# Kernel optimization log

Hardware: AMD Instinct MI355X
Metric: run time of the kernel (lower is better)

## Reference

```python
import jax, jax.numpy as jnp
import numpy as np
from functools import partial

B, S, A = 128, 256, 8
V, E, H, C, HOPS = 50000, 300, 300, 3, 3

def _lstm_dir(x, lens, Wih, Whh, bih, bhh):
    # x: [B,S,E]; masked (packed-style) LSTM: padded steps don't update state, output 0
    b, s, _ = x.shape
    h_dim = Whh.shape[1]
    xg = jnp.einsum('bse,ge->bsg', x, Wih) + bih  # [B,S,4H]
    mask = (jnp.arange(s)[None, :] < lens[:, None])  # [B,S]

    def step(carry, inp):
        h, c = carry
        xg_t, m = inp  # [B,4H], [B]
        g = xg_t + h @ Whh.T + bhh
        i, f, gg, o = jnp.split(g, 4, axis=-1)
        i = jax.nn.sigmoid(i); f = jax.nn.sigmoid(f)
        gg = jnp.tanh(gg); o = jax.nn.sigmoid(o)
        c_new = f * c + i * gg
        h_new = o * jnp.tanh(c_new)
        m2 = m[:, None]
        h2 = jnp.where(m2, h_new, h)
        c2 = jnp.where(m2, c_new, c)
        out = jnp.where(m2, h_new, 0.0)
        return (h2, c2), out

    z = jnp.zeros((b, h_dim), x.dtype)
    _, outs = jax.lax.scan(step, (z, z), (xg.transpose(1, 0, 2), mask.T))
    return outs.transpose(1, 0, 2)

def _bilstm(x, lens, Wih_f, Whh_f, bih_f, bhh_f, Wih_b, Whh_b, bih_b, bhh_b):
    out_f = _lstm_dir(x, lens, Wih_f, Whh_f, bih_f, bhh_f)
    s = x.shape[1]
    t = jnp.arange(s)[None, :]
    # reverse each sequence within its own valid length
    idx = jnp.where(t < lens[:, None], lens[:, None] - 1 - t, t)  # [B,S]
    x_rev = jnp.take_along_axis(x, idx[:, :, None], axis=1)
    out_b_rev = _lstm_dir(x_rev, lens, Wih_b, Whh_b, bih_b, bhh_b)
    out_b = jnp.take_along_axis(out_b_rev, idx[:, :, None], axis=1)
    return jnp.concatenate([out_f, out_b], axis=-1)  # [B,S,2H]

def _locationed_memory(memory, mem_len, left_len, asp_len):
    b, s, _ = memory.shape
    pos = jnp.arange(s, dtype=memory.dtype)[None, :]  # [1,S]
    ml = mem_len[:, None].astype(memory.dtype)
    ll = left_len[:, None].astype(memory.dtype)
    al = asp_len[:, None].astype(memory.dtype)
    in_left = pos < ll
    in_right = (pos >= ll + al) & (pos < ml)
    w = jnp.where(in_left, 1.0 - (ll - pos) / ml,
        jnp.where(in_right, 1.0 - (pos - ll - al + 1.0) / ml, 1.0))
    u = jnp.where(in_left, pos - ll,
        jnp.where(in_right, pos - ll - al + 1.0, 0.0))
    v = memory * w[:, :, None]
    return jnp.concatenate([v, u[:, :, None]], axis=2)  # [B,S,2H+1]

def _gru_cell(x, h, Wih, Whh, bih, bhh):
    gi = x @ Wih.T + bih
    gh = h @ Whh.T + bhh
    i_r, i_z, i_n = jnp.split(gi, 3, axis=-1)
    h_r, h_z, h_n = jnp.split(gh, 3, axis=-1)
    r = jax.nn.sigmoid(i_r + h_r)
    z = jax.nn.sigmoid(i_z + h_z)
    n = jnp.tanh(i_n + r * h_n)
    return (1.0 - z) * n + z * h

def setup_inputs() -> dict:
    key = jax.random.key(0)
    ks = jax.random.split(key, 24)
    mem_len = jax.random.randint(ks[0], (B,), S // 2, S + 1)
    asp_len = jax.random.randint(ks[1], (B,), 1, A + 1)
    max_left = mem_len - asp_len
    left_len = jax.random.randint(ks[2], (B,), 0, 10**6) % (max_left + 1)

    def make_ids(k, n, lens):
        tok = jax.random.randint(k, (B, n), 1, V)
        return jnp.where(jnp.arange(n)[None, :] < lens[:, None], tok, 0)

    text = make_ids(ks[3], S, mem_len)
    aspect = make_ids(ks[4], A, asp_len)
    left_context = make_ids(ks[5], S, left_len)

    def nrm(k, shape, scale=0.05):
        return jax.random.normal(k, shape, jnp.float32) * scale

    params = dict(
        embedding=nrm(ks[6], (V, E), 0.1),
        Wih_f=nrm(ks[7], (4 * H, E)), Whh_f=nrm(ks[8], (4 * H, H)),
        bih_f=nrm(ks[9], (4 * H,)), bhh_f=nrm(ks[10], (4 * H,)),
        Wih_b=nrm(ks[11], (4 * H, E)), Whh_b=nrm(ks[12], (4 * H, H)),
        bih_b=nrm(ks[13], (4 * H,)), bhh_b=nrm(ks[14], (4 * H,)),
        att_W=nrm(ks[15], (1, 2 * H + 1 + 2 * E)), att_b=nrm(ks[16], (1,)),
        gru_Wih=nrm(ks[17], (3 * E, 2 * H + 1)), gru_Whh=nrm(ks[18], (3 * E, E)),
        gru_bih=nrm(ks[19], (3 * E,)), gru_bhh=nrm(ks[20], (3 * E,)),
        dense_W=nrm(ks[21], (C, E)), dense_b=nrm(ks[22], (C,)),
    )
    return dict(text=text, aspect=aspect, left_context=left_context, **params)

def reference(text, aspect, left_context, embedding,
              Wih_f, Whh_f, bih_f, bhh_f, Wih_b, Whh_b, bih_b, bhh_b,
              att_W, att_b, gru_Wih, gru_Whh, gru_bih, gru_bhh,
              dense_W, dense_b):
    left_len = jnp.sum(left_context != 0, axis=-1)
    mem_len = jnp.sum(text != 0, axis=-1)
    asp_len = jnp.sum(aspect != 0, axis=-1)

    memory = embedding[text]  # [B,S,E]
    memory = _bilstm(memory, mem_len, Wih_f, Whh_f, bih_f, bhh_f,
                     Wih_b, Whh_b, bih_b, bhh_b)  # [B,S,2H]
    memory = _locationed_memory(memory, mem_len, left_len, asp_len)  # [B,S,2H+1]

    asp_emb = jnp.sum(embedding[aspect], axis=1) / asp_len[:, None].astype(jnp.float32)  # [B,E]

    et = jnp.zeros_like(asp_emb)
    b, s, _ = memory.shape
    for _ in range(HOPS):
        a = jnp.concatenate([
            memory,
            jnp.broadcast_to(et[:, None, :], (b, s, et.shape[-1])),
            jnp.broadcast_to(asp_emb[:, None, :], (b, s, asp_emb.shape[-1])),
        ], axis=-1)  # [B,S,2H+1+2E]
        g = jnp.einsum('bsd,od->bso', a, att_W) + att_b  # [B,S,1]
        alpha = jax.nn.softmax(g, axis=1)
        i = jnp.einsum('bso,bsd->bd', alpha, memory)  # [B,2H+1]
        et = _gru_cell(i, et, gru_Wih, gru_Whh, gru_bih, gru_bhh)
    return et @ dense_W.T + dense_b  # [B,C]
```

## Files before the change

### kernel.cpp

```cpp
#include <hip/hip_runtime.h>
#include <hip/hip_bf16.h>
#include <math.h>

#define B_ 128
#define S_ 256
#define A_ 8
#define E_ 300
#define H_ 300
#define KPAD 320
#define NGU 16
#define NCOL 80
#define WROW 648
#define HROW 328
#define NBLK 128

typedef unsigned short u16;
typedef unsigned int u32;
typedef unsigned long long u64;
typedef __attribute__((ext_vector_type(8))) short short8;
typedef __attribute__((ext_vector_type(4))) float floatx4;
typedef __attribute__((ext_vector_type(4))) unsigned int u32x4;

#define MFMA16(a, b, c) __builtin_amdgcn_mfma_f32_16x16x32_bf16((a), (b), (c), 0, 0, 0)

__device__ __host__ __forceinline__ int gu_cnt(int g) { return g < 6 ? 20 : 18; }
__device__ __host__ __forceinline__ int gu_u0(int g) { return g < 6 ? 20 * g : 120 + 18 * (g - 6); }

static constexpr size_t oLens = 0;
static constexpr size_t oFlg  = 1536;
static constexpr size_t oH    = 4096;
static constexpr size_t oMemX = 331776;
static constexpr size_t oWp   = 42274816;
static constexpr size_t oBp   = 45551616;
static constexpr size_t oMemV = 45561856;
static constexpr size_t oIT   = 124205056;
static constexpr size_t oGi   = 124512768;
static constexpr size_t oGh   = 124973568;
static constexpr size_t oEt   = 125434368;
static constexpr size_t oSc   = 125587968;
static constexpr size_t oMirr = 125719040;
static constexpr size_t oHL2  = 125721088;
static constexpr size_t WS_NEED = 126048768;

__device__ __forceinline__ u16 f2bf(float f) {
  union { float f; unsigned u; } v; v.f = f;
  unsigned r = (v.u + 0x7FFFu + ((v.u >> 16) & 1u)) >> 16;
  return (u16)r;
}
__device__ __forceinline__ float sigm(float x) { return 1.f / (1.f + __expf(-x)); }
__device__ __forceinline__ float tanh_f(float x) {
  x = fminf(15.f, fmaxf(-15.f, x));
  float e = __expf(2.f * x);
  return (e - 1.f) / (e + 1.f);
}
__device__ __forceinline__ u32 ld_sc0(const u32* p) {
  u32 v;
  asm volatile("global_load_dword %0, %1, off sc0\n\ts_waitcnt vmcnt(0)"
               : "=v"(v) : "v"(p) : "memory");
  return v;
}

__global__ __launch_bounds__(256) void init_kernel(const int* __restrict__ text,
                                                   const int* __restrict__ aspect,
                                                   const int* __restrict__ leftc,
                                                   char* __restrict__ ws) {
  const int bid = blockIdx.x, tid = threadIdx.x;
  if (bid == 0) {
    if (tid < B_) {
      int c = 0; const int* p = text + tid * S_;
      for (int s = 0; s < S_; ++s) c += (p[s] != 0);
      ((int*)(ws + oLens))[tid] = c;
    }
  } else if (bid == 1) {
    if (tid < B_) {
      int c = 0; const int* p = leftc + tid * S_;
      for (int s = 0; s < S_; ++s) c += (p[s] != 0);
      ((int*)(ws + oLens + 512))[tid] = c;
    }
  } else if (bid == 2) {
    if (tid < B_) {
      int c = 0; const int* p = aspect + tid * A_;
      for (int s = 0; s < A_; ++s) c += (p[s] != 0);
      ((int*)(ws + oLens + 1024))[tid] = c;
    }
  } else {
    const int F1 = 512, F2 = 512, HW = 81920, H2 = 81920, EW = 38400;
    const int total = F1 + F2 + HW + H2 + EW;
    for (int i = (bid - 3) * 256 + tid; i < total; i += 64 * 256) {
      int j = i;
      if (j < F1)            { ((u32*)(ws + oFlg))[j] = 0u; continue; }  j -= F1;
      if (j < F2)            { ((u32*)(ws + oMirr))[j] = 0u; continue; } j -= F2;
      if (j < HW)            { ((u32*)(ws + oH))[j] = 0u; continue; }    j -= HW;
      if (j < H2)            { ((u32*)(ws + oHL2))[j] = 0u; continue; }  j -= H2;
      ((u32*)(ws + oEt))[j] = 0u;
    }
  }
}

__global__ __launch_bounds__(256) void pack_kernel(
    const float* __restrict__ WihF, const float* __restrict__ WhhF,
    const float* __restrict__ bihF, const float* __restrict__ bhhF,
    const float* __restrict__ WihB, const float* __restrict__ WhhB,
    const float* __restrict__ bihB, const float* __restrict__ bhhB,
    char* __restrict__ ws) {
  const int WTOT = 2 * NGU * NCOL * 640;
  int idx = blockIdx.x * 256 + threadIdx.x;
  if (idx < WTOT) {
    int k = idx % 640;
    int n = (idx / 640) % NCOL;
    int g = (idx / (640 * NCOL)) % NGU;
    int dir = idx / (640 * NCOL * NGU);
    float v = 0.f;
    const int cnt = gu_cnt(g), u0 = gu_u0(g);
    if (n < cnt * 4) {
      int col = (n & 3) * 300 + u0 + (n >> 2);
      const float* Wih = dir ? WihB : WihF;
      const float* Whh = dir ? WhhB : WhhF;
      if (k < 300)                  v = Wih[(size_t)col * 300 + k];
      else if (k >= 320 && k < 620) v = Whh[(size_t)col * 300 + (k - 320)];
    }
    ((u16*)(ws + oWp))[idx] = f2bf(v);
  } else {
    int j = idx - WTOT;
    if (j < 2 * NGU * NCOL) {
      int n = j % NCOL; int g = (j / NCOL) % NGU; int dir = j / (NCOL * NGU);
      float v = 0.f;
      const int cnt = gu_cnt(g), u0 = gu_u0(g);
      if (n < cnt * 4) {
        int col = (n & 3) * 300 + u0 + (n >> 2);
        v = (dir ? bihB : bihF)[col] + (dir ? bhhB : bhhF)[col];
      }
      ((float*)(ws + oBp))[j] = v;
    }
  }
}

__global__ __launch_bounds__(KPAD) void gather_kernel(const int* __restrict__ text,
                                                      const float* __restrict__ emb,
                                                      char* __restrict__ ws) {
  const int bid = blockIdx.x;
  const int t = bid & 255;
  const int b = (bid >> 8) & 127;
  const int dir = bid >> 15;
  const int len = ((const int*)(ws + oLens))[b];
  const int tp = (dir == 0) ? t : ((t < len) ? (len - 1 - t) : t);
  const int tok = text[b * S_ + tp];
  u16* dst = (u16*)(ws + oMemX) + ((size_t)((dir * B_ + b) * S_ + t)) * KPAD;
  const float* src = emb + (size_t)tok * E_;
  const int k = threadIdx.x;
  float v = (k < E_) ? src[k] : 0.f;
  dst[k] = f2bf(v);
}

__global__ __launch_bounds__(256, 1) void lstm_kernel(char* __restrict__ ws) {
  const int bid = (int)blockIdx.x;
  const int pod = bid & 7;
  const int dir = pod >> 2;
  const int gb  = pod & 3;
  const int g   = bid >> 3;
  const int cnt = gu_cnt(g), u0 = gu_u0(g);
  const int npair = cnt >> 1;
  const int tid = threadIdx.x;
  const int wv = tid >> 6;
  const int lane = tid & 63;
  const int quad = lane >> 4;
  const int l16 = lane & 15;
  const int Mtile = wv >> 1;
  const int nt0 = (wv & 1) ? 3 : 0;
  const int ntc = (wv & 1) ? 2 : 3;

  const u64* __restrict__ Wp64 = (const u64*)(ws + oWp) + (size_t)(dir * NGU + g) * NCOL * 160;
  const float* __restrict__ Bpk = (const float*)(ws + oBp) + (dir * NGU + g) * NCOL;
  const u16* __restrict__ memx = (const u16*)(ws + oMemX) + (size_t)dir * B_ * S_ * KPAD;
  const u16* __restrict__ hb16 = (const u16*)(ws + oH);
  u32* __restrict__ hb32 = (u32*)(ws + oH);
  const u16* __restrict__ hl16 = (const u16*)(ws + oHL2);
  u32* __restrict__ hl32 = (u32*)(ws + oHL2);
  float* __restrict__ memv = (float*)(ws + oMemV);
  u32* __restrict__ flagsP = (u32*)(ws + oFlg) + (size_t)pod * 64;
  u32* __restrict__ flagsM = (u32*)(ws + oMirr) + (size_t)pod * 64;

  __shared__ __align__(16) u16 Wlds[NCOL * WROW];
  __shared__ __align__(16) u16 hLds[32 * HROW];
  __shared__ float gatesLds[32 * 81];
  __shared__ float cS[640];
  __shared__ float hS[640];
  __shared__ float biasS[NCOL];
  __shared__ int lenS[32], llS[32], alS[32];
  __shared__ int remoteS;

  for (int i = tid; i < NCOL * 160; i += 256) {
    int n = i / 160, k4 = i - n * 160;
    ((u64*)Wlds)[n * 162 + k4] = Wp64[i];
  }
  for (int i = tid; i < 640; i += 256) { cS[i] = 0.f; hS[i] = 0.f; }
  if (tid < NCOL) biasS[tid] = Bpk[tid];
  if (tid < 32) {
    lenS[tid] = ((const int*)(ws + oLens))[gb * 32 + tid];
    llS[tid]  = ((const int*)(ws + oLens + 512))[gb * 32 + tid];
    alS[tid]  = ((const int*)(ws + oLens + 1024))[gb * 32 + tid];
  }
  if (tid == 0) remoteS = 0;
  __syncthreads();

  const int row = gb * 32 + Mtile * 16 + l16;
  const u16* wq = Wlds + l16 * WROW + quad * 8;

  int eoff[5]; u16* ldst[5];
  #pragma unroll
  for (int it = 0; it < 5; ++it) {
    int e = (it * 256 + tid) * 8;
    int r = e / KPAD, c = e - r * KPAD;
    eoff[it] = e;
    ldst[it] = hLds + r * HROW + c;
  }
  const u16* hA = hLds + (Mtile * 16 + l16) * HROW + quad * 8;

  short8 xv[10];
  {
    const u16* xr = memx + ((size_t)row * S_) * KPAD + quad * 8;
    #pragma unroll
    for (int kk = 0; kk < 10; ++kk) xv[kk] = *(const short8*)(xr + kk * 32);
  }

  for (int t = 0; t < S_; ++t) {
    if (t > 0) {
      if (wv == 0) {
        const u32 target = (u32)t;
        int spin = 0;
        while (true) {
          u32 f = 0xFFFFFFFFu;
          const int rm = *(volatile int*)&remoteS;
          if (lane < NGU)
            f = rm ? __hip_atomic_load(&flagsM[lane * 4], __ATOMIC_RELAXED, __HIP_MEMORY_SCOPE_AGENT)
                   : ld_sc0(&flagsP[lane * 4]);
          if (__all((int)(f >= target))) break;
          ++spin;
          if (!rm && spin > 64 && (spin & 15) == 0) {
            u32 fm = 0u, fp = 0xFFFFFFFFu;
            if (lane < NGU) {
              fm = __hip_atomic_load(&flagsM[lane * 4], __ATOMIC_RELAXED, __HIP_MEMORY_SCOPE_AGENT);
              fp = ld_sc0(&flagsP[lane * 4]);
            }
            if (__any((int)(fm > fp))) { if (lane == 0) *(volatile int*)&remoteS = 1; }
          }
          if (rm) __builtin_amdgcn_s_sleep(1);
        }
      }
      __syncthreads();
      __builtin_amdgcn_fence(__ATOMIC_ACQUIRE, "workgroup");
    }

    const int rem = *(volatile int*)&remoteS;
    u32x4 hstash[5];
    {
      const size_t pbase = (((size_t)(t & 1) * 2 + dir) * B_ + gb * 32) * KPAD;
      if (rem) {
        const u16* hpan = hb16 + pbase;
        #pragma unroll
        for (int it = 0; it < 5; ++it)
          asm volatile("global_load_dwordx4 %0, %1, off sc1"
                       : "=v"(hstash[it]) : "v"(hpan + eoff[it]) : "memory");
      } else {
        const u16* hpan = hl16 + pbase;
        #pragma unroll
        for (int it = 0; it < 5; ++it)
          asm volatile("global_load_dwordx4 %0, %1, off sc0"
                       : "=v"(hstash[it]) : "v"(hpan + eoff[it]) : "memory");
      }
    }

    floatx4 acc[3];
    acc[0] = (floatx4){0.f, 0.f, 0.f, 0.f}; acc[1] = acc[0]; acc[2] = acc[0];
    #pragma unroll
    for (int kk = 0; kk < 10; ++kk) {
      const int ko = kk * 32;
      #pragma unroll
      for (int j = 0; j < 3; ++j) {
        if (j < ntc)
          acc[j] = MFMA16(xv[kk], *(const short8*)(wq + (nt0 + j) * 16 * WROW + ko), acc[j]);
      }
    }

    asm volatile("s_waitcnt vmcnt(0)" ::: "memory");
    #pragma unroll
    for (int it = 0; it < 5; ++it) *(u32x4*)ldst[it] = hstash[it];
    __syncthreads();

    #pragma unroll
    for (int kk = 0; kk < 10; ++kk) {
      const short8 av = *(const short8*)(hA + kk * 32);
      const int ko = 320 + kk * 32;
      #pragma unroll
      for (int j = 0; j < 3; ++j) {
        if (j < ntc)
          acc[j] = MFMA16(av, *(const short8*)(wq + (nt0 + j) * 16 * WROW + ko), acc[j]);
      }
    }

    #pragma unroll
    for (int j = 0; j < 3; ++j) {
      if (j < ntc) {
        const int colb = (nt0 + j) * 16 + l16;
        const int rb = Mtile * 16 + quad * 4;
        #pragma unroll
        for (int r = 0; r < 4; ++r)
          gatesLds[(rb + r) * 81 + colb] = acc[j][r];
      }
    }
    __syncthreads();

    const int nxt = (t + 1) & 1;
    float2 sv[2]; float* sa[2]; bool sval[2];
    #pragma unroll
    for (int z = 0; z < 2; ++z) {
      const int it = tid + z * 256;
      sval[z] = (it < 32 * npair);
      if (!sval[z]) continue;
      const int bl = it & 31;
      const int pl = it >> 5;
      const int ul0 = pl * 2;
      const int len = lenS[bl];
      const bool m = (t < len);
      const float* gp = gatesLds + bl * 81 + ul0 * 4;
      const float* bp = biasS + ul0 * 4;
      float h0K, h1K, h0N, h1N;
      {
        float ig = sigm(gp[0] + bp[0]);
        float fg = sigm(gp[1] + bp[1]);
        float gt = tanh_f(gp[2] + bp[2]);
        float og = sigm(gp[3] + bp[3]);
        float cOld = cS[ul0 * 32 + bl], hOld = hS[ul0 * 32 + bl];
        float cNew = fg * cOld + ig * gt;
        float hNew = og * tanh_f(cNew);
        cS[ul0 * 32 + bl] = m ? cNew : cOld;
        h0K = m ? hNew : hOld;
        hS[ul0 * 32 + bl] = h0K;
        h0N = m ? hNew : 0.f;
      }
      {
        float ig = sigm(gp[4] + bp[4]);
        float fg = sigm(gp[5] + bp[5]);
        float gt = tanh_f(gp[6] + bp[6]);
        float og = sigm(gp[7] + bp[7]);
        float cOld = cS[(ul0 + 1) * 32 + bl], hOld = hS[(ul0 + 1) * 32 + bl];
        float cNew = fg * cOld + ig * gt;
        float hNew = og * tanh_f(cNew);
        cS[(ul0 + 1) * 32 + bl] = m ? cNew : cOld;
        h1K = m ? hNew : hOld;
        hS[(ul0 + 1) * 32 + bl] = h1K;
        h1N = m ? hNew : 0.f;
      }
      const int bglob = gb * 32 + bl;
      const size_t hidx = (((size_t)nxt * 2 + dir) * B_ + bglob) * 160 + ((u0 + ul0) >> 1);
      u32 packed = (u32)f2bf(h0K) | ((u32)f2bf(h1K) << 16);
      hl32[hidx] = packed;
      __hip_atomic_store(&hb32[hidx], packed,
                         __ATOMIC_RELAXED, __HIP_MEMORY_SCOPE_AGENT);
      int pos = (dir == 0) ? t : (m ? (len - 1 - t) : t);
      float ml = (float)len, ll = (float)llS[bl], al = (float)alS[bl];
      float p = (float)pos;
      float wl;
      if (p < ll) wl = 1.f - (ll - p) / ml;
      else if ((p >= ll + al) && (p < ml)) wl = 1.f - (p - ll - al + 1.f) / ml;
      else wl = 1.f;
      sv[z] = make_float2(h0N * wl, h1N * wl);
      sa[z] = &memv[((size_t)bglob * S_ + pos) * 600 + dir * 300 + u0 + ul0];
    }

    __builtin_amdgcn_fence(__ATOMIC_RELEASE, "workgroup");
    __syncthreads();
    if (tid == 0) {
      *(volatile u32*)&flagsP[g * 4] = (u32)(t + 1);
      __hip_atomic_store(&flagsM[g * 4], (u32)(t + 1),
                         __ATOMIC_RELAXED, __HIP_MEMORY_SCOPE_AGENT);
    }

    #pragma unroll
    for (int z = 0; z < 2; ++z)
      if (sval[z]) *(float2*)sa[z] = sv[z];
    if (t + 1 < S_) {
      const u16* xr = memx + ((size_t)row * S_ + (t + 1)) * KPAD + quad * 8;
      #pragma unroll
      for (int kk = 0; kk < 10; ++kk) xv[kk] = *(const short8*)(xr + kk * 32);
    }
  }
}

__global__ __launch_bounds__(256) void score_kernel(const float* __restrict__ attW,
                                                    char* __restrict__ ws) {
  const int bid = blockIdx.x;
  const int b = bid >> 1, sh = bid & 1;
  const int tid = threadIdx.x, wv = tid >> 6, lane = tid & 63;
  __shared__ float aW[601];
  for (int i = tid; i < 601; i += 256) aW[i] = attW[i];
  const float* memv = (const float*)(ws + oMemV) + (size_t)b * S_ * 600;
  const float ml = (float)((const int*)(ws + oLens))[b];
  const float ll = (float)((const int*)(ws + oLens + 512))[b];
  const float al = (float)((const int*)(ws + oLens + 1024))[b];
  __syncthreads();
  float* scg = (float*)(ws + oSc) + b * S_;
  for (int s = sh * 128 + wv; s < sh * 128 + 128; s += 4) {
    const float* rowp = memv + (size_t)s * 600;
    float acc = 0.f;
    for (int d = lane; d < 600; d += 64) acc += rowp[d] * aW[d];
    for (int off = 32; off; off >>= 1) acc += __shfl_xor(acc, off);
    if (lane == 0) {
      float p = (float)s;
      bool inl = p < ll;
      bool inr = (p >= ll + al) && (p < ml);
      float u = inl ? (p - ll) : (inr ? (p - ll - al + 1.f) : 0.f);
      scg[s] = acc + u * aW[600];
    }
  }
}

__global__ __launch_bounds__(256) void attn_kernel(char* __restrict__ ws) {
  const int bid = blockIdx.x;
  const int b = bid >> 1, dh = bid & 1;
  const int tid = threadIdx.x, wv = tid >> 6, lane = tid & 63;
  __shared__ float alpha[256];
  __shared__ float red[8];
  const float* scg = (const float*)(ws + oSc) + b * S_;
  float v = scg[tid];
  float mx = v;
  for (int off = 32; off; off >>= 1) mx = fmaxf(mx, __shfl_xor(mx, off));
  if (lane == 0) red[wv] = mx;
  __syncthreads();
  mx = fmaxf(fmaxf(red[0], red[1]), fmaxf(red[2], red[3]));
  float e = __expf(v - mx);
  float sm = e;
  for (int off = 32; off; off >>= 1) sm += __shfl_xor(sm, off);
  if (lane == 0) red[4 + wv] = sm;
  __syncthreads();
  float tot = red[4] + red[5] + red[6] + red[7];
  alpha[tid] = e / tot;
  const float ml = (float)((const int*)(ws + oLens))[b];
  const float ll = (float)((const int*)(ws + oLens + 512))[b];
  const float al = (float)((const int*)(ws + oLens + 1024))[b];
  __syncthreads();
  const float* memv = (const float*)(ws + oMemV) + (size_t)b * S_ * 600;
  float* iT = (float*)(ws + oIT);
  const int d0 = dh * 301, d1 = dh ? 601 : 301;
  for (int d = d0 + tid; d < d1; d += 256) {
    float acc = 0.f;
    if (d < 600) {
      for (int s = 0; s < 256; ++s) acc += alpha[s] * memv[(size_t)s * 600 + d];
    } else {
      for (int s = 0; s < 256; ++s) {
        float p = (float)s;
        bool inl = p < ll;
        bool inr = (p >= ll + al) && (p < ml);
        float u = inl ? (p - ll) : (inr ? (p - ll - al + 1.f) : 0.f);
        acc += alpha[s] * u;
      }
    }
    iT[d * 128 + b] = acc;
  }
}

__global__ __launch_bounds__(256) void gi_kernel(const float* __restrict__ Wih,
                                                 const float* __restrict__ bih,
                                                 char* __restrict__ ws) {
  int idx = blockIdx.x * 256 + threadIdx.x;
  int r = idx >> 7, b = idx & 127;
  if (r >= 900) return;
  const float* iT = (const float*)(ws + oIT);
  const float* wr = Wih + (size_t)r * 601;
  float acc = bih[r];
  for (int d = 0; d < 601; ++d) acc += iT[d * 128 + b] * wr[d];
  ((float*)(ws + oGi))[r * 128 + b] = acc;
}

__global__ __launch_bounds__(256) void gh_kernel(const float* __restrict__ Whh,
                                                 const float* __restrict__ bhh,
                                                 char* __restrict__ ws) {
  int idx = blockIdx.x * 256 + threadIdx.x;
  int r = idx >> 7, b = idx & 127;
  if (r >= 900) return;
  const float* et = (const float*)(ws + oEt);
  const float* wr = Whh + (size_t)r * 300;
  float acc = bhh[r];
  for (int u = 0; u < 300; ++u) acc += et[u * 128 + b] * wr[u];
  ((float*)(ws + oGh))[r * 128 + b] = acc;
}

__global__ __launch_bounds__(256) void up_kernel(char* __restrict__ ws) {
  int idx = blockIdx.x * 256 + threadIdx.x;
  int u = idx >> 7, b = idx & 127;
  if (u >= 300) return;
  const float* gi = (const float*)(ws + oGi);
  const float* gh = (const float*)(ws + oGh);
  float* et = (float*)(ws + oEt);
  float rr = sigm(gi[u * 128 + b] + gh[u * 128 + b]);
  float zz = sigm(gi[(300 + u) * 128 + b] + gh[(300 + u) * 128 + b]);
  float nn = tanh_f(gi[(600 + u) * 128 + b] + rr * gh[(600 + u) * 128 + b]);
  float old = et[u * 128 + b];
  et[u * 128 + b] = (1.f - zz) * nn + zz * old;
}

__global__ __launch_bounds__(384) void dense_kernel(const float* __restrict__ dW,
                                                    const float* __restrict__ dB,
                                                    float* __restrict__ out,
                                                    const char* __restrict__ ws) {
  int tid = threadIdx.x;
  if (tid >= 384) return;
  int b = tid / 3, c = tid - 3 * (tid / 3);
  const float* et = (const float*)(ws + oEt);
  float acc = dB[c];
  const float* wr = dW + c * 300;
  for (int u = 0; u < 300; ++u) acc += et[u * 128 + b] * wr[u];
  out[b * 3 + c] = acc;
}

extern "C" void kernel_launch(void* const* d_in, const int* in_sizes, int n_in,
                              void* d_out, int out_size, void* d_ws, size_t ws_size,
                              hipStream_t stream) {
  const int* text = (const int*)d_in[0];
  const int* aspect = (const int*)d_in[1];
  const int* leftc = (const int*)d_in[2];
  const float* emb = (const float*)d_in[3];
  const float* WihF = (const float*)d_in[4];
  const float* WhhF = (const float*)d_in[5];
  const float* bihF = (const float*)d_in[6];
  const float* bhhF = (const float*)d_in[7];
  const float* WihB = (const float*)d_in[8];
  const float* WhhB = (const float*)d_in[9];
  const float* bihB = (const float*)d_in[10];
  const float* bhhB = (const float*)d_in[11];
  const float* attW = (const float*)d_in[12];
  const float* gruWih = (const float*)d_in[14];
  const float* gruWhh = (const float*)d_in[15];
  const float* gruBih = (const float*)d_in[16];
  const float* gruBhh = (const float*)d_in[17];
  const float* denseW = (const float*)d_in[18];
  const float* denseB = (const float*)d_in[19];
  float* out = (float*)d_out;
  char* ws = (char*)d_ws;
  if (ws_size < WS_NEED) return;

  init_kernel<<<67, 256, 0, stream>>>(text, aspect, leftc, ws);
  pack_kernel<<<6420, 256, 0, stream>>>(WihF, WhhF, bihF, bhhF, WihB, WhhB, bihB, bhhB, ws);
  gather_kernel<<<2 * B_ * S_, KPAD, 0, stream>>>(text, emb, ws);
  lstm_kernel<<<NBLK, 256, 0, stream>>>(ws);
  score_kernel<<<2 * B_, 256, 0, stream>>>(attW, ws);
  attn_kernel<<<2 * B_, 256, 0, stream>>>(ws);
  gi_kernel<<<450, 256, 0, stream>>>(gruWih, gruBih, ws);
  for (int h = 0; h < 3; ++h) {
    gh_kernel<<<450, 256, 0, stream>>>(gruWhh, gruBhh, ws);
    up_kernel<<<150, 256, 0, stream>>>(ws);
  }
  dense_kernel<<<1, 384, 0, stream>>>(denseW, denseB, out, ws);
}
```

Baseline: 1.912 ms.

## Replace per-step flag synchronization with step-tagged hidden-state exchange

Removes the separate flag arrays and the flag spin-wait between LSTM recurrence blocks. Each hidden-state word is now written as a 64-bit value carrying the step tag, and consumers poll the data itself until every tag matches, so the release fence, the extra barrier and the flag round trip disappear from each timestep. It also changes the gate LDS stride and replaces __syncthreads with raw barriers. The cost is doubled hidden-state traffic and repeated reloads of whole panels while spinning, and correctness depends on 64-bit stores being seen atomically.

```diff
diff --git a/kernel.cpp b/kernel.cpp
--- a/kernel.cpp
+++ b/kernel.cpp
@@ -13,6 +13,8 @@
 #define WROW 648
 #define HROW 328
 #define NBLK 128
+#define GST 82
+#define PROBE_START 256
 
 typedef unsigned short u16;
 typedef unsigned int u32;
@@ -22,13 +24,12 @@
 typedef __attribute__((ext_vector_type(4))) unsigned int u32x4;
 
 #define MFMA16(a, b, c) __builtin_amdgcn_mfma_f32_16x16x32_bf16((a), (b), (c), 0, 0, 0)
+#define LD4_SC0(d, a) asm volatile("global_load_dwordx4 %0, %1, off sc0" : "=v"(d) : "v"(a) : "memory")
 
 __device__ __host__ __forceinline__ int gu_cnt(int g) { return g < 6 ? 20 : 18; }
 __device__ __host__ __forceinline__ int gu_u0(int g) { return g < 6 ? 20 * g : 120 + 18 * (g - 6); }
 
 static constexpr size_t oLens = 0;
-static constexpr size_t oFlg  = 1536;
-static constexpr size_t oH    = 4096;
 static constexpr size_t oMemX = 331776;
 static constexpr size_t oWp   = 42274816;
 static constexpr size_t oBp   = 45551616;
@@ -38,9 +39,9 @@
 static constexpr size_t oGh   = 124973568;
 static constexpr size_t oEt   = 125434368;
 static constexpr size_t oSc   = 125587968;
-static constexpr size_t oMirr = 125719040;
-static constexpr size_t oHL2  = 125721088;
-static constexpr size_t WS_NEED = 126048768;
+static constexpr size_t oHTP  = 125719040;
+static constexpr size_t oHTS  = 126374400;
+static constexpr size_t WS_NEED = 127029760;
 
 __device__ __forceinline__ u16 f2bf(float f) {
   union { float f; unsigned u; } v; v.f = f;
@@ -53,11 +54,27 @@
   float e = __expf(2.f * x);
   return (e - 1.f) / (e + 1.f);
 }
-__device__ __forceinline__ u32 ld_sc0(const u32* p) {
-  u32 v;
-  asm volatile("global_load_dword %0, %1, off sc0\n\ts_waitcnt vmcnt(0)"
-               : "=v"(v) : "v"(p) : "memory");
-  return v;
+
+__device__ __forceinline__ bool tags_ok(const u32x4 (&q)[10], u32 tgv, int scol0) {
+  bool ok = true;
+  #pragma unroll
+  for (int i = 0; i < 10; ++i) {
+    ok = ok && ((q[i][1] == tgv) || (scol0 + 2 * i >= 150));
+    ok = ok && ((q[i][3] == tgv) || (scol0 + 2 * i + 1 >= 150));
+  }
+  return ok;
+}
+__device__ __forceinline__ void load_plain(u32x4 (&q)[10], const u64* sp) {
+  #pragma unroll
+  for (int i = 0; i < 10; ++i) LD4_SC0(q[i], sp + 2 * i);
+}
+__device__ __forceinline__ void load_mirror(u32x4 (&q)[10], const u64* sp) {
+  #pragma unroll
+  for (int i = 0; i < 10; ++i) {
+    u64 lo = __hip_atomic_load(sp + 2 * i, __ATOMIC_RELAXED, __HIP_MEMORY_SCOPE_AGENT);
+    u64 hi = __hip_atomic_load(sp + 2 * i + 1, __ATOMIC_RELAXED, __HIP_MEMORY_SCOPE_AGENT);
+    q[i] = (u32x4){(u32)lo, (u32)(lo >> 32), (u32)hi, (u32)(hi >> 32)};
+  }
 }
 
 __global__ __launch_bounds__(256) void init_kernel(const int* __restrict__ text,
@@ -84,14 +101,12 @@
       ((int*)(ws + oLens + 1024))[tid] = c;
     }
   } else {
-    const int F1 = 512, F2 = 512, HW = 81920, H2 = 81920, EW = 38400;
-    const int total = F1 + F2 + HW + H2 + EW;
+    const int T1 = 163840, T2 = 163840, EW = 38400;
+    const int total = T1 + T2 + EW;
     for (int i = (bid - 3) * 256 + tid; i < total; i += 64 * 256) {
       int j = i;
-      if (j < F1)            { ((u32*)(ws + oFlg))[j] = 0u; continue; }  j -= F1;
-      if (j < F2)            { ((u32*)(ws + oMirr))[j] = 0u; continue; } j -= F2;
-      if (j < HW)            { ((u32*)(ws + oH))[j] = 0u; continue; }    j -= HW;
-      if (j < H2)            { ((u32*)(ws + oHL2))[j] = 0u; continue; }  j -= H2;
+      if (j < T1)            { ((u32*)(ws + oHTP))[j] = 0u; continue; }  j -= T1;
+      if (j < T2)            { ((u32*)(ws + oHTS))[j] = 0u; continue; }  j -= T2;
       ((u32*)(ws + oEt))[j] = 0u;
     }
   }
@@ -172,17 +187,13 @@
   const u64* __restrict__ Wp64 = (const u64*)(ws + oWp) + (size_t)(dir * NGU + g) * NCOL * 160;
   const float* __restrict__ Bpk = (const float*)(ws + oBp) + (dir * NGU + g) * NCOL;
   const u16* __restrict__ memx = (const u16*)(ws + oMemX) + (size_t)dir * B_ * S_ * KPAD;
-  const u16* __restrict__ hb16 = (const u16*)(ws + oH);
-  u32* __restrict__ hb32 = (u32*)(ws + oH);
-  const u16* __restrict__ hl16 = (const u16*)(ws + oHL2);
-  u32* __restrict__ hl32 = (u32*)(ws + oHL2);
+  u64* __restrict__ hTP = (u64*)(ws + oHTP);
+  u64* __restrict__ hTS = (u64*)(ws + oHTS);
   float* __restrict__ memv = (float*)(ws + oMemV);
-  u32* __restrict__ flagsP = (u32*)(ws + oFlg) + (size_t)pod * 64;
-  u32* __restrict__ flagsM = (u32*)(ws + oMirr) + (size_t)pod * 64;
 
   __shared__ __align__(16) u16 Wlds[NCOL * WROW];
   __shared__ __align__(16) u16 hLds[32 * HROW];
-  __shared__ float gatesLds[32 * 81];
+  __shared__ float gatesLds[32 * GST];
   __shared__ float cS[640];
   __shared__ float hS[640];
   __shared__ float biasS[NCOL];
@@ -194,6 +205,7 @@
     ((u64*)Wlds)[n * 162 + k4] = Wp64[i];
   }
   for (int i = tid; i < 640; i += 256) { cS[i] = 0.f; hS[i] = 0.f; }
+  for (int i = tid; i < 32 * HROW / 2; i += 256) ((u32*)hLds)[i] = 0u;
   if (tid < NCOL) biasS[tid] = Bpk[tid];
   if (tid < 32) {
     lenS[tid] = ((const int*)(ws + oLens))[gb * 32 + tid];
@@ -205,16 +217,12 @@
 
   const int row = gb * 32 + Mtile * 16 + l16;
   const u16* wq = Wlds + l16 * WROW + quad * 8;
-
-  int eoff[5]; u16* ldst[5];
-  #pragma unroll
-  for (int it = 0; it < 5; ++it) {
-    int e = (it * 256 + tid) * 8;
-    int r = e / KPAD, c = e - r * KPAD;
-    eoff[it] = e;
-    ldst[it] = hLds + r * HROW + c;
-  }
   const u16* hA = hLds + (Mtile * 16 + l16) * HROW + quad * 8;
+
+  const int srow = tid >> 3;
+  const int scol0 = (tid & 7) * 20;
+  u16* sdst = hLds + srow * HROW + scol0 * 2;
+  const size_t sboff = ((size_t)dir * B_ + gb * 32 + srow) * 160 + scol0;
 
   short8 xv[10];
   {
@@ -224,50 +232,13 @@
   }
 
   for (int t = 0; t < S_; ++t) {
+    const size_t poff = (size_t)(t & 1) * (2 * B_ * 160) + sboff;
+    u32x4 q[10];
+    int rm0 = 0;
     if (t > 0) {
-      if (wv == 0) {
-        const u32 target = (u32)t;
-        int spin = 0;
-        while (true) {
-          u32 f = 0xFFFFFFFFu;
-          const int rm = *(volatile int*)&remoteS;
-          if (lane < NGU)
-            f = rm ? __hip_atomic_load(&flagsM[lane * 4], __ATOMIC_RELAXED, __HIP_MEMORY_SCOPE_AGENT)
-                   : ld_sc0(&flagsP[lane * 4]);
-          if (__all((int)(f >= target))) break;
-          ++spin;
-          if (!rm && spin > 64 && (spin & 15) == 0) {
-            u32 fm = 0u, fp = 0xFFFFFFFFu;
-            if (lane < NGU) {
-              fm = __hip_atomic_load(&flagsM[lane * 4], __ATOMIC_RELAXED, __HIP_MEMORY_SCOPE_AGENT);
-              fp = ld_sc0(&flagsP[lane * 4]);
-            }
-            if (__any((int)(fm > fp))) { if (lane == 0) *(volatile int*)&remoteS = 1; }
-          }
-          if (rm) __builtin_amdgcn_s_sleep(1);
-        }
-      }
-      __syncthreads();
-      __builtin_amdgcn_fence(__ATOMIC_ACQUIRE, "workgroup");
-    }
-
-    const int rem = *(volatile int*)&remoteS;
-    u32x4 hstash[5];
-    {
-      const size_t pbase = (((size_t)(t & 1) * 2 + dir) * B_ + gb * 32) * KPAD;
-      if (rem) {
-        const u16* hpan = hb16 + pbase;
-        #pragma unroll
-        for (int it = 0; it < 5; ++it)
-          asm volatile("global_load_dwordx4 %0, %1, off sc1"
-                       : "=v"(hstash[it]) : "v"(hpan + eoff[it]) : "memory");
-      } else {
-        const u16* hpan = hl16 + pbase;
-        #pragma unroll
-        for (int it = 0; it < 5; ++it)
-          asm volatile("global_load_dwordx4 %0, %1, off sc0"
-                       : "=v"(hstash[it]) : "v"(hpan + eoff[it]) : "memory");
-      }
+      rm0 = *(volatile int*)&remoteS;
+      if (!rm0) load_plain(q, hTP + poff);
+      else      load_mirror(q, hTS + poff);
     }
 
     floatx4 acc[3];
@@ -282,10 +253,42 @@
       }
     }
 
-    asm volatile("s_waitcnt vmcnt(0)" ::: "memory");
-    #pragma unroll
-    for (int it = 0; it < 5; ++it) *(u32x4*)ldst[it] = hstash[it];
-    __syncthreads();
+    if (t > 0) {
+      const u32 tgv = (u32)t;
+      if (!rm0) {
+        int spin = 0;
+        while (true) {
+          asm volatile("s_waitcnt vmcnt(0)" ::: "memory");
+          __builtin_amdgcn_sched_barrier(0);
+          if (tags_ok(q, tgv, scol0)) break;
+          ++spin;
+          if (spin >= PROBE_START && (spin & 15) == 0) {
+            u32x4 qs[10];
+            load_mirror(qs, hTS + poff);
+            if (tags_ok(qs, tgv, scol0)) {
+              #pragma unroll
+              for (int i = 0; i < 10; ++i) q[i] = qs[i];
+              *(volatile int*)&remoteS = 1;
+              break;
+            }
+          }
+          load_plain(q, hTP + poff);
+        }
+      } else {
+        while (!tags_ok(q, tgv, scol0)) {
+          __builtin_amdgcn_s_sleep(2);
+          load_mirror(q, hTS + poff);
+        }
+      }
+      #pragma unroll
+      for (int i = 0; i < 10; i += 2) {
+        u32x4 pk = (u32x4){q[i][0], q[i][2], q[i + 1][0], q[i + 1][2]};
+        *(u32x4*)(sdst + 4 * i) = pk;
+      }
+    }
+
+    asm volatile("s_waitcnt lgkmcnt(0)" ::: "memory");
+    asm volatile("s_barrier" ::: "memory");
 
     #pragma unroll
     for (int kk = 0; kk < 10; ++kk) {
@@ -305,80 +308,70 @@
         const int rb = Mtile * 16 + quad * 4;
         #pragma unroll
         for (int r = 0; r < 4; ++r)
-          gatesLds[(rb + r) * 81 + colb] = acc[j][r];
-      }
-    }
-    __syncthreads();
-
-    const int nxt = (t + 1) & 1;
-    float2 sv[2]; float* sa[2]; bool sval[2];
+          gatesLds[(rb + r) * GST + colb] = acc[j][r];
+      }
+    }
+    asm volatile("s_waitcnt lgkmcnt(0)" ::: "memory");
+    asm volatile("s_barrier" ::: "memory");
+
     #pragma unroll
     for (int z = 0; z < 2; ++z) {
       const int it = tid + z * 256;
-      sval[z] = (it < 32 * npair);
-      if (!sval[z]) continue;
-      const int bl = it & 31;
-      const int pl = it >> 5;
-      const int ul0 = pl * 2;
-      const int len = lenS[bl];
-      const bool m = (t < len);
-      const float* gp = gatesLds + bl * 81 + ul0 * 4;
-      const float* bp = biasS + ul0 * 4;
-      float h0K, h1K, h0N, h1N;
-      {
-        float ig = sigm(gp[0] + bp[0]);
-        float fg = sigm(gp[1] + bp[1]);
-        float gt = tanh_f(gp[2] + bp[2]);
-        float og = sigm(gp[3] + bp[3]);
-        float cOld = cS[ul0 * 32 + bl], hOld = hS[ul0 * 32 + bl];
-        float cNew = fg * cOld + ig * gt;
-        float hNew = og * tanh_f(cNew);
-        cS[ul0 * 32 + bl] = m ? cNew : cOld;
-        h0K = m ? hNew : hOld;
-        hS[ul0 * 32 + bl] = h0K;
-        h0N = m ? hNew : 0.f;
-      }
-      {
-        float ig = sigm(gp[4] + bp[4]);
-        float fg = sigm(gp[5] + bp[5]);
-        float gt = tanh_f(gp[6] + bp[6]);
-        float og = sigm(gp[7] + bp[7]);
-        float cOld = cS[(ul0 + 1) * 32 + bl], hOld = hS[(ul0 + 1) * 32 + bl];
-        float cNew = fg * cOld + ig * gt;
-        float hNew = og * tanh_f(cNew);
-        cS[(ul0 + 1) * 32 + bl] = m ? cNew : cOld;
-        h1K = m ? hNew : hOld;
-        hS[(ul0 + 1) * 32 + bl] = h1K;
-        h1N = m ? hNew : 0.f;
-      }
-      const int bglob = gb * 32 + bl;
-      const size_t hidx = (((size_t)nxt * 2 + dir) * B_ + bglob) * 160 + ((u0 + ul0) >> 1);
-      u32 packed = (u32)f2bf(h0K) | ((u32)f2bf(h1K) << 16);
-      hl32[hidx] = packed;
-      __hip_atomic_store(&hb32[hidx], packed,
-                         __ATOMIC_RELAXED, __HIP_MEMORY_SCOPE_AGENT);
-      int pos = (dir == 0) ? t : (m ? (len - 1 - t) : t);
-      float ml = (float)len, ll = (float)llS[bl], al = (float)alS[bl];
-      float p = (float)pos;
-      float wl;
-      if (p < ll) wl = 1.f - (ll - p) / ml;
-      else if ((p >= ll + al) && (p < ml)) wl = 1.f - (p - ll - al + 1.f) / ml;
-      else wl = 1.f;
-      sv[z] = make_float2(h0N * wl, h1N * wl);
-      sa[z] = &memv[((size_t)bglob * S_ + pos) * 600 + dir * 300 + u0 + ul0];
-    }
-
-    __builtin_amdgcn_fence(__ATOMIC_RELEASE, "workgroup");
-    __syncthreads();
-    if (tid == 0) {
-      *(volatile u32*)&flagsP[g * 4] = (u32)(t + 1);
-      __hip_atomic_store(&flagsM[g * 4], (u32)(t + 1),
-                         __ATOMIC_RELAXED, __HIP_MEMORY_SCOPE_AGENT);
-    }
-
-    #pragma unroll
-    for (int z = 0; z < 2; ++z)
-      if (sval[z]) *(float2*)sa[z] = sv[z];
+      if (it < 32 * npair) {
+        const int bl = it & 31;
+        const int pl = it >> 5;
+        const int ul0 = pl * 2;
+        const int len = lenS[bl];
+        const bool m = (t < len);
+        const float* gp = gatesLds + bl * GST + ul0 * 4;
+        const float* bp = biasS + ul0 * 4;
+        float h0K, h1K, h0N, h1N;
+        {
+          float ig = sigm(gp[0] + bp[0]);
+          float fg = sigm(gp[1] + bp[1]);
+          float gt = tanh_f(gp[2] + bp[2]);
+          float og = sigm(gp[3] + bp[3]);
+          float cOld = cS[ul0 * 32 + bl], hOld = hS[ul0 * 32 + bl];
+          float cNew = fg * cOld + ig * gt;
+          float hNew = og * tanh_f(cNew);
+          cS[ul0 * 32 + bl] = m ? cNew : cOld;
+          h0K = m ? hNew : hOld;
+          hS[ul0 * 32 + bl] = h0K;
+          h0N = m ? hNew : 0.f;
+        }
+        {
+          float ig = sigm(gp[4] + bp[4]);
+          float fg = sigm(gp[5] + bp[5]);
+          float gt = tanh_f(gp[6] + bp[6]);
+          float og = sigm(gp[7] + bp[7]);
+          float cOld = cS[(ul0 + 1) * 32 + bl], hOld = hS[(ul0 + 1) * 32 + bl];
+          float cNew = fg * cOld + ig * gt;
+          float hNew = og * tanh_f(cNew);
+          cS[(ul0 + 1) * 32 + bl] = m ? cNew : cOld;
+          h1K = m ? hNew : hOld;
+          hS[(ul0 + 1) * 32 + bl] = h1K;
+          h1N = m ? hNew : 0.f;
+        }
+        const int bglob = gb * 32 + bl;
+        u32 packed = (u32)f2bf(h0K) | ((u32)f2bf(h1K) << 16);
+        u64 tg64 = (u64)packed | ((u64)(u32)(t + 1) << 32);
+        const size_t hx = (size_t)((t + 1) & 1) * (2 * B_ * 160)
+                        + ((size_t)dir * B_ + bglob) * 160 + ((u0 + ul0) >> 1);
+        *(volatile u64*)(hTP + hx) = tg64;
+        __hip_atomic_store(&hTS[hx], tg64,
+                           __ATOMIC_RELAXED, __HIP_MEMORY_SCOPE_AGENT);
+        int pos = (dir == 0) ? t : (m ? (len - 1 - t) : t);
+        float ml = (float)len, ll = (float)llS[bl], al = (float)alS[bl];
+        float p = (float)pos;
+        float wl;
+        if (p < ll) wl = 1.f - (ll - p) / ml;
+        else if ((p >= ll + al) && (p < ml)) wl = 1.f - (p - ll - al + 1.f) / ml;
+        else wl = 1.f;
+        *(float2*)&memv[((size_t)bglob * S_ + pos) * 600 + dir * 300 + u0 + ul0] =
+            make_float2(h0N * wl, h1N * wl);
+      }
+    }
+
     if (t + 1 < S_) {
       const u16* xr = memx + ((size_t)row * S_ + (t + 1)) * KPAD + quad * 8;
       #pragma unroll
```

Measured after the change: 4.291 ms. +124.5%, slower.
